# Kernel optimization log

Hardware: AMD Instinct MI355X
Metric: run time of the kernel (lower is better)

The kernel has to match this reference:

```python
import jax, jax.numpy as jnp
import numpy as np

B, S, I, F = 2048, 512, 256, 256  # batch, seq_length, input_size, filter_num


def setup_inputs() -> dict:
    key = jax.random.key(0)
    ks = jax.random.split(key, 9)
    sc = 0.05
    return {
        "hidden": jax.random.normal(ks[0], (B, I), jnp.float32),
        "inp": jax.random.normal(ks[1], (B, S, I), jnp.float32),
        "W1": jax.random.normal(ks[2], (F, I), jnp.float32) * sc,   # linear1 weight (no bias)
        "Wc": jax.random.normal(ks[3], (F, S), jnp.float32) * sc,   # conv kernel [F,1,S,1] squeezed
        "bc": jax.random.normal(ks[4], (F,), jnp.float32) * sc,     # conv bias
        "W2": jax.random.normal(ks[5], (I, I + F), jnp.float32) * sc,
        "b2": jax.random.normal(ks[6], (I,), jnp.float32) * sc,
        "Wfc": jax.random.normal(ks[7], (1, I), jnp.float32) * sc,
        "bfc": jax.random.normal(ks[8], (1,), jnp.float32) * sc,
    }


def reference(hidden, inp, W1, Wc, bc, W2, b2, Wfc, bfc):
    # w = linear1(hidden).unsqueeze(1): [B,1,F]
    w = hidden @ W1.T  # [B,F]
    # Conv2d(1,F,kernel=(S,1)) over input [B,1,S,I] -> [B,F,1,I]; kernel spans full
    # time axis with width 1, so it's a contraction over t per input channel i.
    Hc_raw = jnp.einsum('bti,ft->bfi', inp, Wc) + bc[None, :, None]  # [B,F,I]
    # faithful to torch: .squeeze().reshape([-1, input_size, filter_num])
    H_c = Hc_raw.reshape(-1, I, F)  # [B,I,F]
    s = jnp.sum(H_c * w[:, None, :], axis=2)          # [B,I]
    a = jax.nn.sigmoid(s)
    v = jnp.sum(a[:, :, None] * H_c, axis=1)          # [B,F]
    concat = jnp.concatenate([hidden, v], axis=1)     # [B,I+F]
    h_prime = concat @ W2.T + b2                      # [B,I]
    out = h_prime @ Wfc.T + bfc                       # [B,1]
    return out
```

## Files before the change

### kernel.cpp

```cpp
#include <hip/hip_runtime.h>

#define B_ 2048
#define S_ 512
#define I_ 256
#define F_ 256
#define NG 8

#define OFF_W    0
#define OFF_SW   (OFF_W + B_*F_)
#define OFF_RP   (OFF_SW + B_)
#define OFF_RH   (OFF_RP + NG*512)
#define OFF_RV   (OFF_RH + 256)
#define OFF_SC   (OFF_RV + 256)
#define OFF_U    531456
#define OFF_P    (OFF_U + B_*S_)

__global__ __launch_bounds__(256) void k_pre(
    const float* __restrict__ hidden, const float* __restrict__ W1,
    const float* __restrict__ W2, const float* __restrict__ Wfc,
    float* __restrict__ ws) {
  const int tid = threadIdx.x;

  if (blockIdx.x >= B_ / 4) {
    const int g = blockIdx.x - B_ / 4;
    float acc0 = 0.f, acc1 = 0.f;
#pragma unroll 8
    for (int ii = 0; ii < 32; ++ii) {
      const int i = g * 32 + ii;
      const float f = Wfc[i];
      acc0 += f * W2[(size_t)i * (I_ + F_) + tid];
      acc1 += f * W2[(size_t)i * (I_ + F_) + tid + 256];
    }
    ws[OFF_RP + g * 512 + tid] = acc0;
    ws[OFF_RP + g * 512 + 256 + tid] = acc1;
    return;
  }

  __shared__ float h[4][I_];
  __shared__ float red[256];
  const int b0 = blockIdx.x * 4;
#pragma unroll
  for (int k = 0; k < 4; ++k) h[k][tid] = hidden[(size_t)(b0 + k) * I_ + tid];
  __syncthreads();

  const int f = tid;
  const float4* wrow = (const float4*)(W1 + (size_t)f * I_);
  float acc[4] = {0.f, 0.f, 0.f, 0.f};
#pragma unroll 4
  for (int iq = 0; iq < I_ / 4; ++iq) {
    const float4 v = wrow[iq];
    const int i = 4 * iq;
#pragma unroll
    for (int k = 0; k < 4; ++k)
      acc[k] += v.x * h[k][i] + v.y * h[k][i + 1] + v.z * h[k][i + 2] + v.w * h[k][i + 3];
  }
#pragma unroll
  for (int k = 0; k < 4; ++k) ws[OFF_W + (size_t)(b0 + k) * F_ + f] = acc[k];

#pragma unroll
  for (int k = 0; k < 4; ++k) {
    red[tid] = acc[k];
    __syncthreads();
    for (int s = 128; s > 0; s >>= 1) { if (tid < s) red[tid] += red[tid + s]; __syncthreads(); }
    if (tid == 0) ws[OFF_SW + b0 + k] = red[0];
    __syncthreads();
  }
}

__global__ __launch_bounds__(256) void k_mid(
    const float* __restrict__ Wfc, const float* __restrict__ b2,
    const float* __restrict__ bfc, float* __restrict__ ws) {
  const int tid = threadIdx.x;
  const int lane = tid & 63;
  const int wid = tid >> 6;
  __shared__ float redA[4], redB[4];

  float rh = 0.f, rv = 0.f;
#pragma unroll
  for (int g = 0; g < NG; ++g) {
    rh += ws[OFF_RP + g * 512 + tid];
    rv += ws[OFF_RP + g * 512 + 256 + tid];
  }
  ws[OFF_RH + tid] = rh;
  ws[OFF_RV + tid] = rv;

  float t0 = rv, t1 = Wfc[tid] * b2[tid];
#pragma unroll
  for (int m = 32; m >= 1; m >>= 1) {
    t0 += __shfl_xor(t0, m, 64);
    t1 += __shfl_xor(t1, m, 64);
  }
  if (lane == 0) { redA[wid] = t0; redB[wid] = t1; }
  __syncthreads();
  if (tid == 0) {
    ws[OFF_SC + 0] = redA[0] + redA[1] + redA[2] + redA[3];
    ws[OFF_SC + 1] = redB[0] + redB[1] + redB[2] + redB[3] + bfc[0];
  }
}

__global__ __launch_bounds__(256) void k1_scan(
    const float* __restrict__ inp, const float* __restrict__ wsw,
    const float* __restrict__ wsrv,
    float* __restrict__ wsu, float* __restrict__ wsp) {
  const int ROWS = 32;
  const int b = blockIdx.y;
  const int t0 = blockIdx.x * ROWS;
  const int tid = threadIdx.x;
  const int lane = tid & 63;
  const int wid = tid >> 6;

  const float4 w4  = ((const float4*)(wsw + (size_t)b * F_))[lane];
  const float4 rv4 = ((const float4*)wsrv)[lane];
  const float* base = inp + ((size_t)b * S_ + t0) * I_;
  float* uo = wsu + (size_t)b * S_ + t0;
  float* po = wsp + (size_t)b * S_ + t0;

#pragma unroll
  for (int rr = 0; rr < ROWS / 4; ++rr) {
    const int row = wid + 4 * rr;
    const float4 in4 = ((const float4*)(base + (size_t)row * I_))[lane];
    float du = in4.x * w4.x + in4.y * w4.y + in4.z * w4.z + in4.w * w4.w;
    float dp = in4.x * rv4.x + in4.y * rv4.y + in4.z * rv4.z + in4.w * rv4.w;
#pragma unroll
    for (int m = 32; m >= 1; m >>= 1) {
      du += __shfl_xor(du, m, 64);
      dp += __shfl_xor(dp, m, 64);
    }
    if (lane == 0) { uo[row] = du; po[row] = dp; }
  }
}

__global__ __launch_bounds__(256) void k2_epilogue(
    const float* __restrict__ Wc, const float* __restrict__ bc,
    const float* __restrict__ hidden,
    const float* __restrict__ wsu, const float* __restrict__ wsp,
    const float* __restrict__ wsSw, const float* __restrict__ wsrh,
    const float* __restrict__ wssc, float* __restrict__ out) {
  const int b0 = blockIdx.x * 4;
  const int x = threadIdx.x;
  const int lane = x & 63;
  const int wid = x >> 6;
  __shared__ float wred[4][4];

  const float R  = wssc[0];
  const float c0 = wssc[1];
  const float rh = wsrh[x];

  const float4* wrow = (const float4*)(Wc + (size_t)x * S_);
  const float* ub = wsu + (size_t)b0 * S_;
  const float* pb = wsp + (size_t)b0 * S_;
  float ss[4] = {0.f, 0.f, 0.f, 0.f};
  float qs[4] = {0.f, 0.f, 0.f, 0.f};
#pragma unroll 4
  for (int tq = 0; tq < S_ / 4; ++tq) {
    const float4 v = wrow[tq];
    const int t = 4 * tq;
#pragma unroll
    for (int k = 0; k < 4; ++k) {
      const float4 u4 = *(const float4*)(ub + (size_t)k * S_ + t);
      const float4 p4 = *(const float4*)(pb + (size_t)k * S_ + t);
      ss[k] += v.x * u4.x + v.y * u4.y + v.z * u4.z + v.w * u4.w;
      qs[k] += v.x * p4.x + v.y * p4.y + v.z * p4.z + v.w * p4.w;
    }
  }

  const float bcx = bc[x];
#pragma unroll
  for (int k = 0; k < 4; ++k) {
    const float Sw = wsSw[b0 + k];
    const float s = ss[k] + bcx * Sw;
    const float a = 1.f / (1.f + expf(-s));
    float partial = a * (qs[k] + bcx * R) + rh * hidden[(size_t)(b0 + k) * I_ + x];
#pragma unroll
    for (int m = 32; m >= 1; m >>= 1) partial += __shfl_xor(partial, m, 64);
    if (lane == 0) wred[k][wid] = partial;
  }
  __syncthreads();
  if (x < 4)
    out[b0 + x] = wred[x][0] + wred[x][1] + wred[x][2] + wred[x][3] + c0;
}

extern "C" void kernel_launch(void* const* d_in, const int* in_sizes, int n_in,
                              void* d_out, int out_size, void* d_ws, size_t ws_size,
                              hipStream_t stream) {
  (void)in_sizes; (void)n_in; (void)out_size; (void)ws_size;
  const float* hidden = (const float*)d_in[0];
  const float* inp    = (const float*)d_in[1];
  const float* W1     = (const float*)d_in[2];
  const float* Wc     = (const float*)d_in[3];
  const float* bc     = (const float*)d_in[4];
  const float* W2     = (const float*)d_in[5];
  const float* b2     = (const float*)d_in[6];
  const float* Wfc    = (const float*)d_in[7];
  const float* bfc    = (const float*)d_in[8];
  float* out = (float*)d_out;
  float* ws  = (float*)d_ws;

  hipLaunchKernelGGL(k_pre, dim3(B_ / 4 + NG), dim3(256), 0, stream,
                     hidden, W1, W2, Wfc, ws);
  hipLaunchKernelGGL(k_mid, dim3(1), dim3(256), 0, stream, Wfc, b2, bfc, ws);
  hipLaunchKernelGGL(k1_scan, dim3(S_ / 32, B_), dim3(256), 0, stream,
                     inp, ws + OFF_W, ws + OFF_RV, ws + OFF_U, ws + OFF_P);
  hipLaunchKernelGGL(k2_epilogue, dim3(B_ / 4), dim3(256), 0, stream,
                     Wc, bc, hidden, ws + OFF_U, ws + OFF_P,
                     ws + OFF_SW, ws + OFF_RH, ws + OFF_SC, out);
}
```

Measured before the change: 292.9 us.

## Fuse conv-weight contraction into input scan kernel with atomic accumulation

Transposes Wc into workspace during the pre-kernel and has each scan block contract its 32 time rows against the transposed weights, accumulating per-filter sums into global buffers with atomicAdd. This removes the intermediate u/p arrays and the heavy epilogue loop over the sequence. In exchange it adds a memset of the accumulators and many float atomics, and summation order becomes nondeterministic.

Measured after the change: 264.8 us. 1.11x faster.

```diff
diff --git a/kernel.cpp b/kernel.cpp
--- a/kernel.cpp
+++ b/kernel.cpp
@@ -12,14 +12,36 @@
 #define OFF_RH   (OFF_RP + NG*512)
 #define OFF_RV   (OFF_RH + 256)
 #define OFF_SC   (OFF_RV + 256)
-#define OFF_U    531456
-#define OFF_P    (OFF_U + B_*S_)
+#define OFF_WCT  531456
+#define OFF_SA   (OFF_WCT + S_*F_)
+#define OFF_QA   (OFF_SA + B_*F_)
 
 __global__ __launch_bounds__(256) void k_pre(
     const float* __restrict__ hidden, const float* __restrict__ W1,
     const float* __restrict__ W2, const float* __restrict__ Wfc,
-    float* __restrict__ ws) {
+    const float* __restrict__ Wc, float* __restrict__ ws) {
   const int tid = threadIdx.x;
+
+  if (blockIdx.x >= B_ / 4 + NG) {
+    __shared__ float tile[64][65];
+    const int tt = blockIdx.x - (B_ / 4 + NG);
+    const int x0 = (tt & 3) * 64;
+    const int t0 = (tt >> 2) * 64;
+    const int col = tid & 63;
+    const int wid = tid >> 6;
+#pragma unroll
+    for (int r = 0; r < 16; ++r) {
+      const int row = r * 4 + wid;
+      tile[row][col] = Wc[(size_t)(x0 + row) * S_ + t0 + col];
+    }
+    __syncthreads();
+#pragma unroll
+    for (int r = 0; r < 16; ++r) {
+      const int trow = r * 4 + wid;
+      ws[OFF_WCT + (size_t)(t0 + trow) * F_ + x0 + col] = tile[col][trow];
+    }
+    return;
+  }
 
   if (blockIdx.x >= B_ / 4) {
     const int g = blockIdx.x - B_ / 4;
@@ -98,10 +120,10 @@
   }
 }
 
-__global__ __launch_bounds__(256) void k1_scan(
+__global__ __launch_bounds__(256) void k1_fused(
     const float* __restrict__ inp, const float* __restrict__ wsw,
-    const float* __restrict__ wsrv,
-    float* __restrict__ wsu, float* __restrict__ wsp) {
+    const float* __restrict__ wsrv, const float* __restrict__ wct,
+    float* __restrict__ sacc, float* __restrict__ qacc) {
   const int ROWS = 32;
   const int b = blockIdx.y;
   const int t0 = blockIdx.x * ROWS;
@@ -109,11 +131,12 @@
   const int lane = tid & 63;
   const int wid = tid >> 6;
 
+  __shared__ float u_l[ROWS];
+  __shared__ float p_l[ROWS];
+
   const float4 w4  = ((const float4*)(wsw + (size_t)b * F_))[lane];
   const float4 rv4 = ((const float4*)wsrv)[lane];
   const float* base = inp + ((size_t)b * S_ + t0) * I_;
-  float* uo = wsu + (size_t)b * S_ + t0;
-  float* po = wsp + (size_t)b * S_ + t0;
 
 #pragma unroll
   for (int rr = 0; rr < ROWS / 4; ++rr) {
@@ -126,16 +149,28 @@
       du += __shfl_xor(du, m, 64);
       dp += __shfl_xor(dp, m, 64);
     }
-    if (lane == 0) { uo[row] = du; po[row] = dp; }
-  }
-}
-
-__global__ __launch_bounds__(256) void k2_epilogue(
-    const float* __restrict__ Wc, const float* __restrict__ bc,
-    const float* __restrict__ hidden,
-    const float* __restrict__ wsu, const float* __restrict__ wsp,
+    if (lane == 0) { u_l[row] = du; p_l[row] = dp; }
+  }
+  __syncthreads();
+
+  const float* wcol = wct + (size_t)t0 * F_ + tid;
+  float ss = 0.f, qq = 0.f;
+#pragma unroll 8
+  for (int j = 0; j < ROWS; ++j) {
+    const float w = wcol[(size_t)j * F_];
+    ss += w * u_l[j];
+    qq += w * p_l[j];
+  }
+  atomicAdd(&sacc[(size_t)b * F_ + tid], ss);
+  atomicAdd(&qacc[(size_t)b * F_ + tid], qq);
+}
+
+__global__ __launch_bounds__(256) void k2_small(
+    const float* __restrict__ bc, const float* __restrict__ hidden,
     const float* __restrict__ wsSw, const float* __restrict__ wsrh,
-    const float* __restrict__ wssc, float* __restrict__ out) {
+    const float* __restrict__ wssc,
+    const float* __restrict__ sacc, const float* __restrict__ qacc,
+    float* __restrict__ out) {
   const int b0 = blockIdx.x * 4;
   const int x = threadIdx.x;
   const int lane = x & 63;
@@ -145,32 +180,14 @@
   const float R  = wssc[0];
   const float c0 = wssc[1];
   const float rh = wsrh[x];
-
-  const float4* wrow = (const float4*)(Wc + (size_t)x * S_);
-  const float* ub = wsu + (size_t)b0 * S_;
-  const float* pb = wsp + (size_t)b0 * S_;
-  float ss[4] = {0.f, 0.f, 0.f, 0.f};
-  float qs[4] = {0.f, 0.f, 0.f, 0.f};
-#pragma unroll 4
-  for (int tq = 0; tq < S_ / 4; ++tq) {
-    const float4 v = wrow[tq];
-    const int t = 4 * tq;
-#pragma unroll
-    for (int k = 0; k < 4; ++k) {
-      const float4 u4 = *(const float4*)(ub + (size_t)k * S_ + t);
-      const float4 p4 = *(const float4*)(pb + (size_t)k * S_ + t);
-      ss[k] += v.x * u4.x + v.y * u4.y + v.z * u4.z + v.w * u4.w;
-      qs[k] += v.x * p4.x + v.y * p4.y + v.z * p4.z + v.w * p4.w;
-    }
-  }
-
   const float bcx = bc[x];
+
 #pragma unroll
   for (int k = 0; k < 4; ++k) {
-    const float Sw = wsSw[b0 + k];
-    const float s = ss[k] + bcx * Sw;
+    const float s = sacc[(size_t)(b0 + k) * F_ + x] + bcx * wsSw[b0 + k];
     const float a = 1.f / (1.f + expf(-s));
-    float partial = a * (qs[k] + bcx * R) + rh * hidden[(size_t)(b0 + k) * I_ + x];
+    float partial = a * (qacc[(size_t)(b0 + k) * F_ + x] + bcx * R)
+                  + rh * hidden[(size_t)(b0 + k) * I_ + x];
 #pragma unroll
     for (int m = 32; m >= 1; m >>= 1) partial += __shfl_xor(partial, m, 64);
     if (lane == 0) wred[k][wid] = partial;
@@ -196,12 +213,15 @@
   float* out = (float*)d_out;
   float* ws  = (float*)d_ws;
 
-  hipLaunchKernelGGL(k_pre, dim3(B_ / 4 + NG), dim3(256), 0, stream,
-                     hidden, W1, W2, Wfc, ws);
+  hipMemsetAsync(ws + OFF_SA, 0, 2ull * B_ * F_ * sizeof(float), stream);
+
+  hipLaunchKernelGGL(k_pre, dim3(B_ / 4 + NG + 32), dim3(256), 0, stream,
+                     hidden, W1, W2, Wfc, Wc, ws);
   hipLaunchKernelGGL(k_mid, dim3(1), dim3(256), 0, stream, Wfc, b2, bfc, ws);
-  hipLaunchKernelGGL(k1_scan, dim3(S_ / 32, B_), dim3(256), 0, stream,
-                     inp, ws + OFF_W, ws + OFF_RV, ws + OFF_U, ws + OFF_P);
-  hipLaunchKernelGGL(k2_epilogue, dim3(B_ / 4), dim3(256), 0, stream,
-                     Wc, bc, hidden, ws + OFF_U, ws + OFF_P,
-                     ws + OFF_SW, ws + OFF_RH, ws + OFF_SC, out);
-}
+  hipLaunchKernelGGL(k1_fused, dim3(S_ / 32, B_), dim3(256), 0, stream,
+                     inp, ws + OFF_W, ws + OFF_RV, ws + OFF_WCT,
+                     ws + OFF_SA, ws + OFF_QA);
+  hipLaunchKernelGGL(k2_small, dim3(B_ / 4), dim3(256), 0, stream,
+                     bc, hidden, ws + OFF_SW, ws + OFF_RH, ws + OFF_SC,
+                     ws + OFF_SA, ws + OFF_QA, out);
+}
```
